# Kernel tuning notes

Measured on AMD Instinct MI355X. Metric: run time of the kernel, lower is better.

## Reference

```python
import jax, jax.numpy as jnp
import numpy as np

# --- Izhikevich RS parameters (standard) ---
A, B, C, D = 0.02, 0.2, -65.0, 8.0
V_PEAK = 30.0
DT = 1.0            # Euler step per substep
I_TONIC = -2.0      # pop.i_tonic.fill_(-2.0)
NOISE_STD = 0.3
RATE_DECAY = 0.95   # exponential spike-rate trace (assumed IzhikevichLayer.rate)

SUBSTEPS = 1000
N_CH = 8


def setup_inputs() -> dict:
    key = jax.random.key(0)
    k1, k2, k3 = jax.random.split(key, 3)
    return {
        "retinal_type_L": jax.random.uniform(k1, (400,), dtype=jnp.float32),
        "retinal_type_R": jax.random.uniform(k2, (400,), dtype=jnp.float32),
        # per-substep noise for the 4 populations (uv, blue, green, red)
        "noise": jax.random.normal(k3, (SUBSTEPS, 4, N_CH), dtype=jnp.float32),
        "substeps": SUBSTEPS,
    }


def _drives(type_all):
    food = jnp.sum((type_all > 0.7).astype(jnp.float32))
    enemy = jnp.sum((jnp.abs(type_all - 0.5) < 0.1).astype(jnp.float32))
    rock = jnp.sum((jnp.abs(type_all - 0.75) < 0.1).astype(jnp.float32))
    consp = jnp.sum((jnp.abs(type_all - 0.25) < 0.1).astype(jnp.float32))
    total = food + enemy + rock + consp + 1e-8
    uv = (food * 0.1 + enemy * 0.05 + consp * 0.8 + rock * 0.2) / total
    bl = (food * 0.2 + enemy * 0.1 + consp * 0.5 + rock * 0.3) / total
    gr = (food * 0.8 + enemy * 0.3 + consp * 0.3 + rock * 0.3) / total
    rd = (food * 0.4 + enemy * 0.7 + consp * 0.2 + rock * 0.3) / total
    return jnp.stack([uv, bl, gr, rd])  # (4,)


def reference(retinal_type_L, retinal_type_R, noise, substeps):
    n_ch = noise.shape[-1]
    drives = _drives(jnp.concatenate([retinal_type_L, retinal_type_R]))
    # input current per population, broadcast over neurons: (4, n_ch)
    I_base = drives[:, None] * 10.0 + I_TONIC + jnp.zeros((4, n_ch), noise.dtype)

    v0 = jnp.full((4, n_ch), C, dtype=noise.dtype)
    u0 = B * v0
    r0 = jnp.zeros((4, n_ch), dtype=noise.dtype)

    def step(carry, eps):
        v, u, rate = carry
        I = I_base + eps * NOISE_STD
        v_new = v + DT * (0.04 * v * v + 5.0 * v + 140.0 - u + I)
        u_new = u + DT * A * (B * v - u)
        spike = (v_new >= V_PEAK).astype(v.dtype)
        v_out = jnp.where(spike > 0, C, v_new)
        u_out = u_new + spike * D
        rate = RATE_DECAY * rate + (1.0 - RATE_DECAY) * spike
        return (v_out, u_out, rate), None

    (v, u, rate), _ = jax.lax.scan(step, (v0, u0, r0), noise)

    pop_means = rate.mean(axis=1)  # (4,) -> uv, blue, green, red
    uv_m, bl_m, gr_m, rd_m = pop_means[0], pop_means[1], pop_means[2], pop_means[3]
    rg_opp = rd_m - gr_m
    by_opp = (uv_m + bl_m) / 2.0 - (gr_m + rd_m) / 2.0
    return jnp.stack([uv_m, bl_m, gr_m, rd_m, rg_opp, by_opp])
```

## Files before the change

### kernel.cpp

```cpp
#include <hip/hip_runtime.h>
#include <math.h>


#define FSTEP(eps) do {                                  \
    float I3_ = __builtin_fmaf(0.3f, (eps), Ib140);      \
    float d3_ = __builtin_fmaf(-0.004f, U, I3_);         \
    float w_  = __builtin_fmaf(0.04f, v, 6.0f);          \
    float Un_ = __builtin_fmaf(0.98f, U, v);             \
    float vn_ = __builtin_fmaf(w_, v, d3_);              \
    bool  sp_ = (vn_ >= 30.0f);                          \
    float sv_ = sp_ ? 1.0f : 0.0f;                       \
    v = sp_ ? -65.0f : vn_;                              \
    U = __builtin_fmaf(2000.0f, sv_, Un_);               \
    R = __builtin_fmaf(0.95f, R, sv_);                   \
  } while (0)

#define LOAD16(B, base) do {                             \
    B##0  = (base)[0*32];  B##1  = (base)[1*32];         \
    B##2  = (base)[2*32];  B##3  = (base)[3*32];         \
    B##4  = (base)[4*32];  B##5  = (base)[5*32];         \
    B##6  = (base)[6*32];  B##7  = (base)[7*32];         \
    B##8  = (base)[8*32];  B##9  = (base)[9*32];         \
    B##10 = (base)[10*32]; B##11 = (base)[11*32];        \
    B##12 = (base)[12*32]; B##13 = (base)[13*32];        \
    B##14 = (base)[14*32]; B##15 = (base)[15*32];        \
  } while (0)

#define STEP16(B) do {                                   \
    FSTEP(B##0);  FSTEP(B##1);  FSTEP(B##2);  FSTEP(B##3);   \
    FSTEP(B##4);  FSTEP(B##5);  FSTEP(B##6);  FSTEP(B##7);   \
    FSTEP(B##8);  FSTEP(B##9);  FSTEP(B##10); FSTEP(B##11);  \
    FSTEP(B##12); FSTEP(B##13); FSTEP(B##14); FSTEP(B##15);  \
  } while (0)

__global__ __launch_bounds__(64) void scv_kernel(
    const float* __restrict__ retL, const float* __restrict__ retR,
    const float* __restrict__ noise, float* __restrict__ out, int S) {
  const int lane = threadIdx.x;
  const int neuron = lane & 31;

  float Ib140;
  {
#pragma clang fp contract(off)
    float f = 0.0f, e = 0.0f, r = 0.0f, cp = 0.0f;
    for (int i = lane; i < 800; i += 64) {
      float t = (i < 400) ? retL[i] : retR[i - 400];
      f  += (t > 0.7f) ? 1.0f : 0.0f;
      e  += (fabsf(t - 0.5f)  < 0.1f) ? 1.0f : 0.0f;
      r  += (fabsf(t - 0.75f) < 0.1f) ? 1.0f : 0.0f;
      cp += (fabsf(t - 0.25f) < 0.1f) ? 1.0f : 0.0f;
    }
#pragma unroll
    for (int off = 1; off < 64; off <<= 1) {
      f  += __shfl_xor(f,  off);
      e  += __shfl_xor(e,  off);
      r  += __shfl_xor(r,  off);
      cp += __shfl_xor(cp, off);
    }
    float total = f + e + r + cp + 1e-8f;
    int p = (lane >> 3) & 3;
    float dv;
    if (p == 0)      dv = (f * 0.1f + e * 0.05f + cp * 0.8f + r * 0.2f) / total;
    else if (p == 1) dv = (f * 0.2f + e * 0.1f  + cp * 0.5f + r * 0.3f) / total;
    else if (p == 2) dv = (f * 0.8f + e * 0.3f  + cp * 0.3f + r * 0.3f) / total;
    else             dv = (f * 0.4f + e * 0.7f  + cp * 0.2f + r * 0.3f) / total;
    float Ib = dv * 10.0f + (-2.0f);
    Ib140 = Ib + 140.0f;
  }

  float v = -65.0f;
  float U = -3250.0f;
  float R = 0.0f;

  const float* p = noise + neuron;
  float c0,c1,c2,c3,c4,c5,c6,c7,c8,c9,c10,c11,c12,c13,c14,c15;
  float n0,n1,n2,n3,n4,n5,n6,n7,n8,n9,n10,n11,n12,n13,n14,n15;

  int t = 0;
  if (S >= 48) {
    LOAD16(c, p); p += 16 * 32;
    for (; t + 48 <= S; t += 32) {
      LOAD16(n, p); p += 16 * 32;
      STEP16(c);
      LOAD16(c, p); p += 16 * 32;
      STEP16(n);
    }
    STEP16(c);
    t += 16;
  }
  {
    const float* q = noise + neuron;
    float cur = (t < S) ? q[(size_t)t * 32] : 0.0f;
    for (; t < S; ++t) {
      float nxt = (t + 1 < S) ? q[(size_t)(t + 1) * 32] : 0.0f;
      FSTEP(cur);
      cur = nxt;
    }
  }

  {
#pragma clang fp contract(off)
    float rate = 0.05f * R;
    float rsum = rate;
    rsum += __shfl_xor(rsum, 1);
    rsum += __shfl_xor(rsum, 2);
    rsum += __shfl_xor(rsum, 4);
    float mean = rsum / 8.0f;
    float m_uv = __shfl(mean, 0);
    float m_bl = __shfl(mean, 8);
    float m_gr = __shfl(mean, 16);
    float m_rd = __shfl(mean, 24);
    if (lane == 0) {
      out[0] = m_uv;
      out[1] = m_bl;
      out[2] = m_gr;
      out[3] = m_rd;
      out[4] = m_rd - m_gr;
      out[5] = (m_uv + m_bl) / 2.0f - (m_gr + m_rd) / 2.0f;
    }
  }
}

extern "C" void kernel_launch(void* const* d_in, const int* in_sizes, int n_in,
                              void* d_out, int out_size, void* d_ws,
                              size_t ws_size, hipStream_t stream) {
  const float* retL  = (const float*)d_in[0];
  const float* retR  = (const float*)d_in[1];
  const float* noise = (const float*)d_in[2];
  float* out = (float*)d_out;
  (void)n_in; (void)out_size; (void)d_ws; (void)ws_size;

  const int S = in_sizes[2] / 32;
  hipLaunchKernelGGL(scv_kernel, dim3(1), dim3(64), 0, stream, retL, retR,
                     noise, out, S);
}
```

Baseline: 34.64 us.

## Pack spike bits per step and fold the rate trace through a lookup table

Each Euler step no longer updates the exponential rate trace. A spike bit is shifted into a 32-bit word with v_addc inside inline asm, and the spike test plus the v/U resets use cmp/cndmask with a precomputed U+2000. Every 32 steps the word is folded into R using a 256-entry shared-memory table of 0.95 powers and constant 0.95^8 and 0.95^32 factors. The aim is to cut per-step instructions on the serial single-wave chain. In exchange it adds LDS lookups, inline asm that limits compiler scheduling, and a summation order that changes floating-point rounding.

```diff
diff --git a/kernel.cpp b/kernel.cpp
--- a/kernel.cpp
+++ b/kernel.cpp
@@ -2,35 +2,51 @@
 #include <math.h>
 
 
-#define FSTEP(eps) do {                                  \
-    float I3_ = __builtin_fmaf(0.3f, (eps), Ib140);      \
-    float d3_ = __builtin_fmaf(-0.004f, U, I3_);         \
-    float w_  = __builtin_fmaf(0.04f, v, 6.0f);          \
-    float Un_ = __builtin_fmaf(0.98f, U, v);             \
-    float vn_ = __builtin_fmaf(w_, v, d3_);              \
-    bool  sp_ = (vn_ >= 30.0f);                          \
-    float sv_ = sp_ ? 1.0f : 0.0f;                       \
-    v = sp_ ? -65.0f : vn_;                              \
-    U = __builtin_fmaf(2000.0f, sv_, Un_);               \
-    R = __builtin_fmaf(0.95f, R, sv_);                   \
+#define FSTEP(eps) do {                                          \
+    float I3_ = __builtin_fmaf(0.3f, (eps), Ib140);              \
+    float d3_ = __builtin_fmaf(-0.004f, U, I3_);                 \
+    float w_  = __builtin_fmaf(0.04f, v, 6.0f);                  \
+    float Un_ = __builtin_fmaf(0.98f, U, v);                     \
+    float U8_ = Un_ + 2000.0f;                                   \
+    float vn_ = __builtin_fmaf(w_, v, d3_);                      \
+    float vo_, Uo_;                                              \
+    asm("v_cmp_ge_f32 vcc, %3, %5\n\t"                           \
+        "v_cndmask_b32 %0, %3, %6, vcc\n\t"                      \
+        "v_cndmask_b32 %1, %4, %7, vcc\n\t"                      \
+        "v_addc_co_u32 %2, vcc, %2, %2, vcc"                     \
+        : "=&v"(vo_), "=&v"(Uo_), "+v"(B)                        \
+        : "v"(vn_), "v"(Un_), "v"(c30), "v"(c65), "v"(U8_)       \
+        : "vcc");                                                \
+    v = vo_; U = Uo_;                                            \
   } while (0)
 
-#define LOAD16(B, base) do {                             \
-    B##0  = (base)[0*32];  B##1  = (base)[1*32];         \
-    B##2  = (base)[2*32];  B##3  = (base)[3*32];         \
-    B##4  = (base)[4*32];  B##5  = (base)[5*32];         \
-    B##6  = (base)[6*32];  B##7  = (base)[7*32];         \
-    B##8  = (base)[8*32];  B##9  = (base)[9*32];         \
-    B##10 = (base)[10*32]; B##11 = (base)[11*32];        \
-    B##12 = (base)[12*32]; B##13 = (base)[13*32];        \
-    B##14 = (base)[14*32]; B##15 = (base)[15*32];        \
+#define FOLD32(word) do {                                        \
+    float t0_ = Tsh[(word) & 255u];                              \
+    float t1_ = Tsh[((word) >> 8) & 255u];                       \
+    float t2_ = Tsh[((word) >> 16) & 255u];                      \
+    float t3_ = Tsh[(word) >> 24];                               \
+    float W_  = __builtin_fmaf(C8, t3_, t2_);                    \
+    W_ = __builtin_fmaf(C8, W_, t1_);                            \
+    W_ = __builtin_fmaf(C8, W_, t0_);                            \
+    R  = __builtin_fmaf(C32, R, W_);                             \
   } while (0)
 
-#define STEP16(B) do {                                   \
-    FSTEP(B##0);  FSTEP(B##1);  FSTEP(B##2);  FSTEP(B##3);   \
-    FSTEP(B##4);  FSTEP(B##5);  FSTEP(B##6);  FSTEP(B##7);   \
-    FSTEP(B##8);  FSTEP(B##9);  FSTEP(B##10); FSTEP(B##11);  \
-    FSTEP(B##12); FSTEP(B##13); FSTEP(B##14); FSTEP(B##15);  \
+#define LOAD16(Bf, base) do {                                    \
+    Bf##0  = (base)[0*32];  Bf##1  = (base)[1*32];               \
+    Bf##2  = (base)[2*32];  Bf##3  = (base)[3*32];               \
+    Bf##4  = (base)[4*32];  Bf##5  = (base)[5*32];               \
+    Bf##6  = (base)[6*32];  Bf##7  = (base)[7*32];               \
+    Bf##8  = (base)[8*32];  Bf##9  = (base)[9*32];               \
+    Bf##10 = (base)[10*32]; Bf##11 = (base)[11*32];              \
+    Bf##12 = (base)[12*32]; Bf##13 = (base)[13*32];              \
+    Bf##14 = (base)[14*32]; Bf##15 = (base)[15*32];              \
+  } while (0)
+
+#define STEP16(Bf) do {                                          \
+    FSTEP(Bf##0);  FSTEP(Bf##1);  FSTEP(Bf##2);  FSTEP(Bf##3);   \
+    FSTEP(Bf##4);  FSTEP(Bf##5);  FSTEP(Bf##6);  FSTEP(Bf##7);   \
+    FSTEP(Bf##8);  FSTEP(Bf##9);  FSTEP(Bf##10); FSTEP(Bf##11);  \
+    FSTEP(Bf##12); FSTEP(Bf##13); FSTEP(Bf##14); FSTEP(Bf##15);  \
   } while (0)
 
 __global__ __launch_bounds__(64) void scv_kernel(
@@ -38,6 +54,25 @@
     const float* __restrict__ noise, float* __restrict__ out, int S) {
   const int lane = threadIdx.x;
   const int neuron = lane & 31;
+
+  __shared__ float Tsh[256];
+  {
+    const float W95[8] = {1.0f, 0.95f, 0.9025f, 0.857375f, 0.81450625f,
+                          0.7737809375f, 0.735091890625f, 0.69833729609375f};
+    for (int e = lane; e < 256; e += 64) {
+      float val = 0.0f;
+#pragma unroll
+      for (int i = 0; i < 8; ++i)
+        val += (e & (1 << i)) ? W95[i] : 0.0f;
+      Tsh[e] = val;
+    }
+  }
+  __syncthreads();
+
+  const float C8a = 0.9025f * 0.9025f;
+  const float C8  = C8a * C8a;
+  const float C16 = C8 * C8;
+  const float C32 = C16 * C16;
 
   float Ib140;
   {
@@ -71,22 +106,30 @@
   float v = -65.0f;
   float U = -3250.0f;
   float R = 0.0f;
+  unsigned int B = 0u;
+  unsigned int Bp = 0u;
+  const float c30 = 30.0f, c65 = -65.0f;
 
   const float* p = noise + neuron;
   float c0,c1,c2,c3,c4,c5,c6,c7,c8,c9,c10,c11,c12,c13,c14,c15;
   float n0,n1,n2,n3,n4,n5,n6,n7,n8,n9,n10,n11,n12,n13,n14,n15;
 
   int t = 0;
+  int bits = 0;
   if (S >= 48) {
     LOAD16(c, p); p += 16 * 32;
     for (; t + 48 <= S; t += 32) {
       LOAD16(n, p); p += 16 * 32;
+      FOLD32(Bp);
       STEP16(c);
       LOAD16(c, p); p += 16 * 32;
       STEP16(n);
+      Bp = B; B = 0u;
     }
+    FOLD32(Bp); Bp = 0u;
     STEP16(c);
     t += 16;
+    bits = 16;
   }
   {
     const float* q = noise + neuron;
@@ -95,7 +138,20 @@
       float nxt = (t + 1 < S) ? q[(size_t)(t + 1) * 32] : 0.0f;
       FSTEP(cur);
       cur = nxt;
+      if (++bits == 32) { FOLD32(B); B = 0u; bits = 0; }
     }
+  }
+  {
+    float t0_ = Tsh[B & 255u];
+    float t1_ = Tsh[(B >> 8) & 255u];
+    float t2_ = Tsh[(B >> 16) & 255u];
+    float t3_ = Tsh[B >> 24];
+    float W_  = __builtin_fmaf(C8, t3_, t2_);
+    W_ = __builtin_fmaf(C8, W_, t1_);
+    W_ = __builtin_fmaf(C8, W_, t0_);
+    float pscale = 1.0f;
+    for (int i = 0; i < bits; ++i) pscale *= 0.95f;
+    R = __builtin_fmaf(pscale, R, W_);
   }
 
   {
```

New measurement: 34.97 us. No clear change (+1.0%).
